# Kernel optimization log

Hardware: AMD Instinct MI355X
Metric: run time of the kernel (lower is better)

Reference implementation:

```python
import jax, jax.numpy as jnp
import numpy as np

N = 65536
IN_FEAT = 512
OUT_FEAT = 512
K = 16


def setup_inputs() -> dict:
    key = jax.random.key(0)
    k_feat, k_wt, k_wp, k_idx = jax.random.split(key, 4)
    feat = jax.random.normal(k_feat, (N, IN_FEAT), dtype=jnp.float32)
    # nn.Linear(in, out, bias=False): y = x @ W.T with W [out, in].
    # We store W as [in, out] so y = x @ W (same math, transposed layout).
    scale = 1.0 / np.sqrt(IN_FEAT)
    W_theta = jax.random.uniform(k_wt, (IN_FEAT, OUT_FEAT), dtype=jnp.float32, minval=-scale, maxval=scale)
    W_phi = jax.random.uniform(k_wp, (IN_FEAT, OUT_FEAT), dtype=jnp.float32, minval=-scale, maxval=scale)
    src_ind = jax.random.randint(k_idx, (N, K), 0, N, dtype=jnp.int64)
    return {"k": K, "src_ind": src_ind, "feat": feat, "W_theta": W_theta, "W_phi": W_phi}


def reference(k, src_ind, feat, W_theta, W_phi):
    # Dense projections (cuBLAS-friendly part)
    h_theta = feat @ W_theta            # [N, out]
    h_phi = feat @ W_phi                # [N, out]
    h_src = h_theta                     # message contribution from source node
    h_dst = h_phi - h_theta             # per-destination additive term
    # fused_edgeconv_op: result[i] = max_{j in 0..k} (h_src[src_ind[i, j]] + h_dst[i]).
    # h_dst[i] is constant over neighbors, so max commutes with the add:
    neigh = h_src[src_ind[:, :k]]       # [N, k, out] irregular gather
    result = jnp.max(neigh, axis=1) + h_dst  # [N, out]
    return result
```

## Files before the change

kernel.cpp:

```cpp
#include <hip/hip_runtime.h>
#include <hip/hip_bf16.h>
#include <stdint.h>


typedef __bf16 bf16x8 __attribute__((ext_vector_type(8)));
typedef float f32x4 __attribute__((ext_vector_type(4)));

__device__ __forceinline__ unsigned short f2bf(float x) {
    unsigned u = __float_as_uint(x);
    unsigned r = u + 0x7fffu + ((u >> 16) & 1u);
    return (unsigned short)(r >> 16);
}

__device__ __forceinline__ void async_ld16(const void* g, void* l) {
    __builtin_amdgcn_global_load_lds(
        (const __attribute__((address_space(1))) unsigned int*)g,
        (__attribute__((address_space(3))) unsigned int*)l,
        16, 0, 0);
}

__global__ void k_convert_feat(const float* __restrict__ feat,
                               unsigned short* __restrict__ featb) {
    int i = (blockIdx.x * 256 + threadIdx.x) * 4;
    f32x4 f = __builtin_nontemporal_load((const f32x4*)(feat + i));
    ushort4 o;
    o.x = f2bf(f.x); o.y = f2bf(f.y); o.z = f2bf(f.z); o.w = f2bf(f.w);
    *(ushort4*)(featb + i) = o;
}

__global__ void k_prep_w(const float* __restrict__ Wth,
                         const float* __restrict__ Wph,
                         unsigned short* __restrict__ wtc) {
    __shared__ float tile[32][33];
    const int k0 = (blockIdx.x & 15) * 32;
    const int n0 = (blockIdx.x >> 4) * 32;
    const int t  = threadIdx.x;
    const int cc = t & 31;
    const int r0 = t >> 5;
#pragma unroll
    for (int it = 0; it < 4; ++it) {
        const int r  = it * 8 + r0;
        const int gn = n0 + cc;
        float v;
        if (gn < 512) v = Wth[(k0 + r) * 512 + gn];
        else          v = Wph[(k0 + r) * 512 + (gn - 512)] - Wth[(k0 + r) * 512 + (gn - 512)];
        tile[r][cc] = v;
    }
    __syncthreads();
#pragma unroll
    for (int it = 0; it < 4; ++it) {
        const int r2 = t & 31;
        const int c2 = it * 8 + (t >> 5);
        wtc[(size_t)(n0 + c2) * 512 + k0 + r2] = f2bf(tile[r2][c2]);
    }
}

__global__ void k_gemm(const unsigned short* __restrict__ A,
                       const unsigned short* __restrict__ Bt,
                       unsigned short* __restrict__ theta,
                       float* __restrict__ delta_f,
                       size_t slabStride)
{
    __shared__ __align__(16) unsigned short As[128 * 32];
    __shared__ __align__(16) unsigned short Bs[128 * 32];

    const int tid  = threadIdx.x;
    const int wave = tid >> 6;
    const int lane = tid & 63;
    const int quad = lane >> 4;
    const int l15  = lane & 15;

    const int b  = blockIdx.x;
    const int mt = (b >> 6) * 8 + (b & 7);
    const int nt = (b >> 3) & 7;
    const int m0 = mt * 128;
    const int n0 = nt * 128;

    const int wm = wave >> 1;
    const int wn = wave & 1;

    f32x4 acc[4][4];
#pragma unroll
    for (int i = 0; i < 4; i++)
#pragma unroll
        for (int j = 0; j < 4; j++) acc[i][j] = (f32x4){0.f, 0.f, 0.f, 0.f};

    const int r0   = (wave * 2 + 0) * 16 + (lane >> 2);
    const int r1   = (wave * 2 + 1) * 16 + (lane >> 2);
    const int koff = (lane & 3) * 8;

    const unsigned short* Ag0 = A  + (size_t)(m0 + r0) * 512 + koff;
    const unsigned short* Ag1 = A  + (size_t)(m0 + r1) * 512 + koff;
    const unsigned short* Bg0 = Bt + (size_t)(n0 + r0) * 512 + koff;
    const unsigned short* Bg1 = Bt + (size_t)(n0 + r1) * 512 + koff;

    unsigned short* lA0 = &As[(wave * 2 + 0) * 512];
    unsigned short* lA1 = &As[(wave * 2 + 1) * 512];
    unsigned short* lB0 = &Bs[(wave * 2 + 0) * 512];
    unsigned short* lB1 = &Bs[(wave * 2 + 1) * 512];

    for (int kt = 0; kt < 16; ++kt) {
        const int kg = kt * 32;
        __syncthreads();
        async_ld16(Ag0 + kg, lA0);
        async_ld16(Ag1 + kg, lA1);
        async_ld16(Bg0 + kg, lB0);
        async_ld16(Bg1 + kg, lB1);
        __syncthreads();

        bf16x8 af[4], bfr[4];
#pragma unroll
        for (int t = 0; t < 4; ++t) {
            const int am = wm * 64 + t * 16 + l15;
            af[t]  = *(const bf16x8*)&As[am * 32 + quad * 8];
            const int bn = wn * 64 + t * 16 + l15;
            bfr[t] = *(const bf16x8*)&Bs[bn * 32 + quad * 8];
        }
#pragma unroll
        for (int i = 0; i < 4; i++)
#pragma unroll
            for (int j = 0; j < 4; j++)
                acc[i][j] = __builtin_amdgcn_mfma_f32_16x16x32_bf16(af[i], bfr[j], acc[i][j], 0, 0, 0);
    }

    const bool is_theta = (n0 < 512);
#pragma unroll
    for (int i = 0; i < 4; i++) {
        const int mrow = m0 + wm * 64 + i * 16 + quad * 4;
#pragma unroll
        for (int j = 0; j < 4; j++) {
            const int ncol = n0 + wn * 64 + j * 16 + l15;
#pragma unroll
            for (int r = 0; r < 4; r++) {
                const float v = acc[i][j][r];
                if (is_theta) {
                    theta[(size_t)(ncol >> 5) * slabStride
                          + (size_t)(mrow + r) * 32 + (ncol & 31)] = f2bf(v);
                } else {
                    delta_f[(size_t)(mrow + r) * 512 + (ncol - 512)] = v;
                }
            }
        }
    }
}

__global__ void k_gather(const unsigned short* __restrict__ theta,
                         float* out,
                         const int* __restrict__ src,
                         const int* __restrict__ kptr,
                         int chunksPerSlice, size_t slabStride)
{
    const int b     = blockIdx.x;
    const int xcd   = b & 7;
    const int t2    = b >> 3;
    const int chunk = t2 % chunksPerSlice;
    const int phase = t2 / chunksPerSlice;
    const int slice = phase * 8 + xcd;
    const int kk    = *kptr;

    const unsigned short* slab = theta + (size_t)slice * slabStride;
    const int tid = threadIdx.x;
    const int c8  = (tid & 3) * 8;
    const int rly = tid >> 2;

#pragma unroll 2
    for (int pass = 0; pass < 8; ++pass) {
        const int row = chunk * 512 + pass * 64 + rly;

        float m0 = -INFINITY, m1 = -INFINITY, m2 = -INFINITY, m3 = -INFINITY;
        float m4 = -INFINITY, m5 = -INFINITY, m6 = -INFINITY, m7 = -INFINITY;

        if (kk == 16) {
            const int4* sp = (const int4*)(src + (size_t)row * 16);
            int4 sv[4];
            sv[0] = sp[0]; sv[1] = sp[1]; sv[2] = sp[2]; sv[3] = sp[3];
#pragma unroll
            for (int q = 0; q < 4; ++q) {
                const int ss[4] = {sv[q].x, sv[q].y, sv[q].z, sv[q].w};
#pragma unroll
                for (int j = 0; j < 4; ++j) {
                    const uint4 v = *(const uint4*)(slab + (size_t)ss[j] * 32 + c8);
                    m0 = fmaxf(m0, __uint_as_float(v.x << 16));
                    m1 = fmaxf(m1, __uint_as_float(v.x & 0xffff0000u));
                    m2 = fmaxf(m2, __uint_as_float(v.y << 16));
                    m3 = fmaxf(m3, __uint_as_float(v.y & 0xffff0000u));
                    m4 = fmaxf(m4, __uint_as_float(v.z << 16));
                    m5 = fmaxf(m5, __uint_as_float(v.z & 0xffff0000u));
                    m6 = fmaxf(m6, __uint_as_float(v.w << 16));
                    m7 = fmaxf(m7, __uint_as_float(v.w & 0xffff0000u));
                }
            }
        } else {
            for (int k = 0; k < kk; ++k) {
                const int s = src[(size_t)row * 16 + k];
                const uint4 v = *(const uint4*)(slab + (size_t)s * 32 + c8);
                m0 = fmaxf(m0, __uint_as_float(v.x << 16));
                m1 = fmaxf(m1, __uint_as_float(v.x & 0xffff0000u));
                m2 = fmaxf(m2, __uint_as_float(v.y << 16));
                m3 = fmaxf(m3, __uint_as_float(v.y & 0xffff0000u));
                m4 = fmaxf(m4, __uint_as_float(v.z << 16));
                m5 = fmaxf(m5, __uint_as_float(v.z & 0xffff0000u));
                m6 = fmaxf(m6, __uint_as_float(v.w << 16));
                m7 = fmaxf(m7, __uint_as_float(v.w & 0xffff0000u));
            }
        }

        float* op = out + (size_t)row * 512 + slice * 32 + c8;
        const f32x4 d0 = __builtin_nontemporal_load((const f32x4*)op);
        const f32x4 d1 = __builtin_nontemporal_load((const f32x4*)op + 1);
        f32x4 o0, o1;
        o0[0] = m0 + d0[0]; o0[1] = m1 + d0[1]; o0[2] = m2 + d0[2]; o0[3] = m3 + d0[3];
        o1[0] = m4 + d1[0]; o1[1] = m5 + d1[1]; o1[2] = m6 + d1[2]; o1[3] = m7 + d1[3];
        __builtin_nontemporal_store(o0, (f32x4*)op);
        __builtin_nontemporal_store(o1, (f32x4*)op + 1);
    }
}

extern "C" void kernel_launch(void* const* d_in, const int* in_sizes, int n_in,
                              void* d_out, int out_size, void* d_ws, size_t ws_size,
                              hipStream_t stream) {
    const int*   kptr = (const int*)d_in[0];
    const int*   src  = (const int*)d_in[1];
    const float* feat = (const float*)d_in[2];
    const float* Wth  = (const float*)d_in[3];
    const float* Wph  = (const float*)d_in[4];
    float* out = (float*)d_out;

    const int N = in_sizes[2] / 512;
    const size_t slabStride = (size_t)N * 32;

    unsigned short* featb = (unsigned short*)d_ws;
    unsigned short* wtc   = (unsigned short*)((char*)d_ws + (size_t)64 * 1024 * 1024);
    unsigned short* table = (unsigned short*)((char*)d_ws + (size_t)65 * 1024 * 1024);

    const int chunksPerSlice = N / 512;

    k_convert_feat<<<(N * 512) / 1024, 256, 0, stream>>>(feat, featb);
    k_prep_w<<<512, 256, 0, stream>>>(Wth, Wph, wtc);
    k_gemm<<<(N / 128) * 8, 256, 0, stream>>>(featb, wtc, table, out, slabStride);
    k_gather<<<16 * chunksPerSlice, 256, 0, stream>>>(table, out, src, kptr,
                                                      chunksPerSlice, slabStride);
}
```

Before: 461.9 us.

## Double-buffer GEMM LDS tiles, vectorize epilogue stores, and reshape gather grid

The GEMM now prefetches the next K-tile into a second LDS buffer while MFMAs run on the current one, which removes one barrier per iteration, and it sets launch bounds. The MFMA operand order is swapped so each lane holds four consecutive output columns, letting the epilogue write ushort4 and float4 vectors instead of scalar stores. The gather kernel is restructured so each block covers 256 rows across two slices, keeping the XCD-to-slice mapping but changing the grid shape. The extra LDS buffer lowers the occupancy ceiling, and the per-block work in the gather changes.

```diff
diff --git a/kernel.cpp b/kernel.cpp
--- a/kernel.cpp
+++ b/kernel.cpp
@@ -55,14 +55,15 @@
     }
 }
 
-__global__ void k_gemm(const unsigned short* __restrict__ A,
-                       const unsigned short* __restrict__ Bt,
-                       unsigned short* __restrict__ theta,
-                       float* __restrict__ delta_f,
-                       size_t slabStride)
+__global__ __launch_bounds__(256, 3)
+void k_gemm(const unsigned short* __restrict__ A,
+            const unsigned short* __restrict__ Bt,
+            unsigned short* __restrict__ theta,
+            float* __restrict__ delta_f,
+            size_t slabStride)
 {
-    __shared__ __align__(16) unsigned short As[128 * 32];
-    __shared__ __align__(16) unsigned short Bs[128 * 32];
+    __shared__ __align__(16) unsigned short As[2][128 * 32];
+    __shared__ __align__(16) unsigned short Bs[2][128 * 32];
 
     const int tid  = threadIdx.x;
     const int wave = tid >> 6;
@@ -94,51 +95,60 @@
     const unsigned short* Bg0 = Bt + (size_t)(n0 + r0) * 512 + koff;
     const unsigned short* Bg1 = Bt + (size_t)(n0 + r1) * 512 + koff;
 
-    unsigned short* lA0 = &As[(wave * 2 + 0) * 512];
-    unsigned short* lA1 = &As[(wave * 2 + 1) * 512];
-    unsigned short* lB0 = &Bs[(wave * 2 + 0) * 512];
-    unsigned short* lB1 = &Bs[(wave * 2 + 1) * 512];
-
+    unsigned short* const sA = &As[0][0];
+    unsigned short* const sB = &Bs[0][0];
+    const int oA0 = (wave * 2 + 0) * 512;
+    const int oA1 = (wave * 2 + 1) * 512;
+
+#define STAGE(buf, kg) do {                              \
+        async_ld16(Ag0 + (kg), sA + (buf) * 4096 + oA0); \
+        async_ld16(Ag1 + (kg), sA + (buf) * 4096 + oA1); \
+        async_ld16(Bg0 + (kg), sB + (buf) * 4096 + oA0); \
+        async_ld16(Bg1 + (kg), sB + (buf) * 4096 + oA1); \
+    } while (0)
+
+    STAGE(0, 0);
+    __syncthreads();
+
+#pragma unroll
     for (int kt = 0; kt < 16; ++kt) {
-        const int kg = kt * 32;
-        __syncthreads();
-        async_ld16(Ag0 + kg, lA0);
-        async_ld16(Ag1 + kg, lA1);
-        async_ld16(Bg0 + kg, lB0);
-        async_ld16(Bg1 + kg, lB1);
-        __syncthreads();
+        const int cur = kt & 1;
+        if (kt < 15) STAGE(cur ^ 1, (kt + 1) * 32);
 
         bf16x8 af[4], bfr[4];
 #pragma unroll
         for (int t = 0; t < 4; ++t) {
             const int am = wm * 64 + t * 16 + l15;
-            af[t]  = *(const bf16x8*)&As[am * 32 + quad * 8];
+            af[t]  = *(const bf16x8*)&sA[cur * 4096 + am * 32 + quad * 8];
             const int bn = wn * 64 + t * 16 + l15;
-            bfr[t] = *(const bf16x8*)&Bs[bn * 32 + quad * 8];
+            bfr[t] = *(const bf16x8*)&sB[cur * 4096 + bn * 32 + quad * 8];
         }
 #pragma unroll
         for (int i = 0; i < 4; i++)
 #pragma unroll
             for (int j = 0; j < 4; j++)
-                acc[i][j] = __builtin_amdgcn_mfma_f32_16x16x32_bf16(af[i], bfr[j], acc[i][j], 0, 0, 0);
-    }
+                acc[i][j] = __builtin_amdgcn_mfma_f32_16x16x32_bf16(bfr[j], af[i], acc[i][j], 0, 0, 0);
+
+        if (kt < 15) __syncthreads();
+    }
+#undef STAGE
 
     const bool is_theta = (n0 < 512);
 #pragma unroll
     for (int i = 0; i < 4; i++) {
-        const int mrow = m0 + wm * 64 + i * 16 + quad * 4;
+        const int m = m0 + wm * 64 + i * 16 + l15;
 #pragma unroll
         for (int j = 0; j < 4; j++) {
-            const int ncol = n0 + wn * 64 + j * 16 + l15;
-#pragma unroll
-            for (int r = 0; r < 4; r++) {
-                const float v = acc[i][j][r];
-                if (is_theta) {
-                    theta[(size_t)(ncol >> 5) * slabStride
-                          + (size_t)(mrow + r) * 32 + (ncol & 31)] = f2bf(v);
-                } else {
-                    delta_f[(size_t)(mrow + r) * 512 + (ncol - 512)] = v;
-                }
+            const int nb = n0 + wn * 64 + j * 16 + quad * 4;
+            const f32x4 v = acc[i][j];
+            if (is_theta) {
+                ushort4 o;
+                o.x = f2bf(v[0]); o.y = f2bf(v[1]);
+                o.z = f2bf(v[2]); o.w = f2bf(v[3]);
+                *(ushort4*)&theta[(size_t)(nb >> 5) * slabStride
+                                  + (size_t)m * 32 + (nb & 31)] = o;
+            } else {
+                *(f32x4*)&delta_f[(size_t)m * 512 + (nb - 512)] = v;
             }
         }
     }
@@ -148,38 +158,52 @@
                          float* out,
                          const int* __restrict__ src,
                          const int* __restrict__ kptr,
-                         int chunksPerSlice, size_t slabStride)
+                         size_t slabStride)
 {
     const int b     = blockIdx.x;
     const int xcd   = b & 7;
-    const int t2    = b >> 3;
-    const int chunk = t2 % chunksPerSlice;
-    const int phase = t2 / chunksPerSlice;
-    const int slice = phase * 8 + xcd;
+    const int chunk = b >> 3;
     const int kk    = *kptr;
 
-    const unsigned short* slab = theta + (size_t)slice * slabStride;
     const int tid = threadIdx.x;
     const int c8  = (tid & 3) * 8;
     const int rly = tid >> 2;
 
+    for (int half = 0; half < 2; ++half) {
+        const int slice = half * 8 + xcd;
+        const unsigned short* slab = theta + (size_t)slice * slabStride;
+
 #pragma unroll 2
-    for (int pass = 0; pass < 8; ++pass) {
-        const int row = chunk * 512 + pass * 64 + rly;
-
-        float m0 = -INFINITY, m1 = -INFINITY, m2 = -INFINITY, m3 = -INFINITY;
-        float m4 = -INFINITY, m5 = -INFINITY, m6 = -INFINITY, m7 = -INFINITY;
-
-        if (kk == 16) {
-            const int4* sp = (const int4*)(src + (size_t)row * 16);
-            int4 sv[4];
-            sv[0] = sp[0]; sv[1] = sp[1]; sv[2] = sp[2]; sv[3] = sp[3];
-#pragma unroll
-            for (int q = 0; q < 4; ++q) {
-                const int ss[4] = {sv[q].x, sv[q].y, sv[q].z, sv[q].w};
-#pragma unroll
-                for (int j = 0; j < 4; ++j) {
-                    const uint4 v = *(const uint4*)(slab + (size_t)ss[j] * 32 + c8);
+        for (int pass = 0; pass < 4; ++pass) {
+            const int row = chunk * 256 + pass * 64 + rly;
+
+            float m0 = -INFINITY, m1 = -INFINITY, m2 = -INFINITY, m3 = -INFINITY;
+            float m4 = -INFINITY, m5 = -INFINITY, m6 = -INFINITY, m7 = -INFINITY;
+
+            if (kk == 16) {
+                const int4* sp = (const int4*)(src + (size_t)row * 16);
+                int4 sv[4];
+                sv[0] = sp[0]; sv[1] = sp[1]; sv[2] = sp[2]; sv[3] = sp[3];
+#pragma unroll
+                for (int q = 0; q < 4; ++q) {
+                    const int ss[4] = {sv[q].x, sv[q].y, sv[q].z, sv[q].w};
+#pragma unroll
+                    for (int j = 0; j < 4; ++j) {
+                        const uint4 v = *(const uint4*)(slab + (size_t)ss[j] * 32 + c8);
+                        m0 = fmaxf(m0, __uint_as_float(v.x << 16));
+                        m1 = fmaxf(m1, __uint_as_float(v.x & 0xffff0000u));
+                        m2 = fmaxf(m2, __uint_as_float(v.y << 16));
+                        m3 = fmaxf(m3, __uint_as_float(v.y & 0xffff0000u));
+                        m4 = fmaxf(m4, __uint_as_float(v.z << 16));
+                        m5 = fmaxf(m5, __uint_as_float(v.z & 0xffff0000u));
+                        m6 = fmaxf(m6, __uint_as_float(v.w << 16));
+                        m7 = fmaxf(m7, __uint_as_float(v.w & 0xffff0000u));
+                    }
+                }
+            } else {
+                for (int k = 0; k < kk; ++k) {
+                    const int s = src[(size_t)row * 16 + k];
+                    const uint4 v = *(const uint4*)(slab + (size_t)s * 32 + c8);
                     m0 = fmaxf(m0, __uint_as_float(v.x << 16));
                     m1 = fmaxf(m1, __uint_as_float(v.x & 0xffff0000u));
                     m2 = fmaxf(m2, __uint_as_float(v.y << 16));
@@ -190,29 +214,16 @@
                     m7 = fmaxf(m7, __uint_as_float(v.w & 0xffff0000u));
                 }
             }
-        } else {
-            for (int k = 0; k < kk; ++k) {
-                const int s = src[(size_t)row * 16 + k];
-                const uint4 v = *(const uint4*)(slab + (size_t)s * 32 + c8);
-                m0 = fmaxf(m0, __uint_as_float(v.x << 16));
-                m1 = fmaxf(m1, __uint_as_float(v.x & 0xffff0000u));
-                m2 = fmaxf(m2, __uint_as_float(v.y << 16));
-                m3 = fmaxf(m3, __uint_as_float(v.y & 0xffff0000u));
-                m4 = fmaxf(m4, __uint_as_float(v.z << 16));
-                m5 = fmaxf(m5, __uint_as_float(v.z & 0xffff0000u));
-                m6 = fmaxf(m6, __uint_as_float(v.w << 16));
-                m7 = fmaxf(m7, __uint_as_float(v.w & 0xffff0000u));
-            }
+
+            float* op = out + (size_t)row * 512 + slice * 32 + c8;
+            const f32x4 d0 = __builtin_nontemporal_load((const f32x4*)op);
+            const f32x4 d1 = __builtin_nontemporal_load((const f32x4*)op + 1);
+            f32x4 o0, o1;
+            o0[0] = m0 + d0[0]; o0[1] = m1 + d0[1]; o0[2] = m2 + d0[2]; o0[3] = m3 + d0[3];
+            o1[0] = m4 + d1[0]; o1[1] = m5 + d1[1]; o1[2] = m6 + d1[2]; o1[3] = m7 + d1[3];
+            __builtin_nontemporal_store(o0, (f32x4*)op);
+            __builtin_nontemporal_store(o1, (f32x4*)op + 1);
         }
-
-        float* op = out + (size_t)row * 512 + slice * 32 + c8;
-        const f32x4 d0 = __builtin_nontemporal_load((const f32x4*)op);
-        const f32x4 d1 = __builtin_nontemporal_load((const f32x4*)op + 1);
-        f32x4 o0, o1;
-        o0[0] = m0 + d0[0]; o0[1] = m1 + d0[1]; o0[2] = m2 + d0[2]; o0[3] = m3 + d0[3];
-        o1[0] = m4 + d1[0]; o1[1] = m5 + d1[1]; o1[2] = m6 + d1[2]; o1[3] = m7 + d1[3];
-        __builtin_nontemporal_store(o0, (f32x4*)op);
-        __builtin_nontemporal_store(o1, (f32x4*)op + 1);
     }
 }
 
@@ -233,11 +244,8 @@
     unsigned short* wtc   = (unsigned short*)((char*)d_ws + (size_t)64 * 1024 * 1024);
     unsigned short* table = (unsigned short*)((char*)d_ws + (size_t)65 * 1024 * 1024);
 
-    const int chunksPerSlice = N / 512;
-
     k_convert_feat<<<(N * 512) / 1024, 256, 0, stream>>>(feat, featb);
     k_prep_w<<<512, 256, 0, stream>>>(Wth, Wph, wtc);
     k_gemm<<<(N / 128) * 8, 256, 0, stream>>>(featb, wtc, table, out, slabStride);
-    k_gather<<<16 * chunksPerSlice, 256, 0, stream>>>(table, out, src, kptr,
-                                                      chunksPerSlice, slabStride);
-}
+    k_gather<<<8 * (N / 256), 256, 0, stream>>>(table, out, src, kptr, slabStride);
+}
```

Result: slower. 489.9 us (+6.1%).
